# Performance work log

Measured on AMD Instinct MI355X. Metric: run time of the kernel, lower is better.

The kernel has to match this reference:

```python
import jax, jax.numpy as jnp
import numpy as np

VOCAB, D_MODEL, N_STATE, H_HEADS, LAYERS = 64, 512, 32, 16, 4
EXPAND = 2
D_INNER = EXPAND * D_MODEL          # 1024
P_HEAD = D_INNER // H_HEADS         # 64
CONV_DIM = D_INNER + 2 * N_STATE    # x, B, C share the depthwise conv
K_CONV = 4
D_IN_PROJ = 2 * D_INNER + 2 * N_STATE + H_HEADS  # z, x, B, C, dt
BATCH, SEQ = 4, 1024
EPS = 1e-5


def rmsnorm(x, w):
    return x * jax.lax.rsqrt(jnp.mean(x * x, axis=-1, keepdims=True) + EPS) * w


def silu(x):
    return x * jax.nn.sigmoid(x)


def causal_depthwise_conv(x, w, b):
    # x: [B,L,C], w: [C,K], b: [C]; causal (left) padding, depthwise groups
    xt = jnp.transpose(x, (0, 2, 1))  # [B,C,L]
    out = jax.lax.conv_general_dilated(xt, w[:, None, :], (1,), [(K_CONV - 1, 0)], feature_group_count=w.shape[0])
    return jnp.transpose(out, (0, 2, 1)) + b


def ssd(xh, dt, A, Bm, Cm, Dp):
    # Mamba2 SSD recurrence. xh [B,L,H,P], dt [B,L,H], A [H], Bm/Cm [B,L,N], Dp [H]
    dA = jnp.exp(dt * A)              # decay per (batch, step, head)
    dtx = dt[..., None] * xh          # [B,L,H,P]

    def step(h, inp):
        dA_t, dtx_t, B_t, C_t = inp
        # h: [B,H,P,N]
        h = dA_t[:, :, None, None] * h + dtx_t[..., None] * B_t[:, None, None, :]
        y = jnp.einsum('bhpn,bn->bhp', h, C_t)
        return h, y

    h0 = jnp.zeros((xh.shape[0], H_HEADS, P_HEAD, N_STATE), xh.dtype)
    _, ys = jax.lax.scan(step, h0, (jnp.moveaxis(dA, 1, 0), jnp.moveaxis(dtx, 1, 0), jnp.moveaxis(Bm, 1, 0), jnp.moveaxis(Cm, 1, 0)))
    return jnp.moveaxis(ys, 0, 1) + xh * Dp[None, None, :, None]


def mamba_block(x, norm_w, W_in, b_in, conv_w, conv_b, dt_bias, A_log, Dp, gnorm_w, W_out, b_out):
    res = x
    u = rmsnorm(x, norm_w)
    zxbcdt = u @ W_in + b_in                                # [B,L,D_IN_PROJ]
    z = zxbcdt[..., :D_INNER]
    xBC = zxbcdt[..., D_INNER:D_INNER + CONV_DIM]
    dt = zxbcdt[..., D_INNER + CONV_DIM:]                   # [B,L,H]
    xBC = silu(causal_depthwise_conv(xBC, conv_w, conv_b))
    xc = xBC[..., :D_INNER]
    Bm = xBC[..., D_INNER:D_INNER + N_STATE]
    Cm = xBC[..., D_INNER + N_STATE:]
    dt = jax.nn.softplus(dt + dt_bias)
    xh = xc.reshape(xc.shape[0], xc.shape[1], H_HEADS, P_HEAD)
    y = ssd(xh, dt, -jnp.exp(A_log), Bm, Cm, Dp)
    y = y.reshape(y.shape[0], y.shape[1], D_INNER)
    y = rmsnorm(y * silu(z), gnorm_w)                       # gated RMSNorm
    return res + y @ W_out + b_out


def forward(input_tokens, emb, norm_w, W_in, b_in, conv_w, conv_b, dt_bias, A_log, D_param, gnorm_w, W_out, b_out, head_w, head_b):
    h = emb[input_tokens]
    for i in range(LAYERS):
        h = mamba_block(h, norm_w[i], W_in[i], b_in[i], conv_w[i], conv_b[i], dt_bias[i], A_log[i], D_param[i], gnorm_w[i], W_out[i], b_out[i])
    return h @ head_w + head_b


def setup_inputs() -> dict:
    key = jax.random.key(0)
    ks = jax.random.split(key, 8)
    s = 0.02
    return {
        'input_tokens': jax.random.randint(ks[0], (BATCH, SEQ), 0, VOCAB),
        'emb': jax.random.normal(ks[1], (VOCAB, D_MODEL), jnp.float32) * s,
        'norm_w': jnp.ones((LAYERS, D_MODEL), jnp.float32),
        'W_in': jax.random.normal(ks[2], (LAYERS, D_MODEL, D_IN_PROJ), jnp.float32) * s,
        'b_in': jnp.zeros((LAYERS, D_IN_PROJ), jnp.float32),
        'conv_w': jax.random.normal(ks[3], (LAYERS, CONV_DIM, K_CONV), jnp.float32) * 0.1,
        'conv_b': jnp.zeros((LAYERS, CONV_DIM), jnp.float32),
        'dt_bias': jnp.tile(jnp.log(jnp.expm1(jnp.linspace(0.001, 0.1, H_HEADS, dtype=jnp.float32))), (LAYERS, 1)),
        'A_log': jnp.tile(jnp.log(jnp.arange(1, H_HEADS + 1, dtype=jnp.float32)), (LAYERS, 1)),
        'D_param': jnp.ones((LAYERS, H_HEADS), jnp.float32),
        'gnorm_w': jnp.ones((LAYERS, D_INNER), jnp.float32),
        'W_out': jax.random.normal(ks[4], (LAYERS, D_INNER, D_MODEL), jnp.float32) * s,
        'b_out': jnp.zeros((LAYERS, D_MODEL), jnp.float32),
        'head_w': jax.random.normal(ks[5], (D_MODEL, VOCAB), jnp.float32) * s,
        'head_b': jnp.zeros((VOCAB,), jnp.float32),
    }


def reference(input_tokens, emb, norm_w, W_in, b_in, conv_w, conv_b, dt_bias, A_log, D_param, gnorm_w, W_out, b_out, head_w, head_b):
    return forward(input_tokens, emb, norm_w, W_in, b_in, conv_w, conv_b, dt_bias, A_log, D_param, gnorm_w, W_out, b_out, head_w, head_b)
```

## Files before the change

### kernel.cpp

```cpp
#include <hip/hip_runtime.h>
#include <hip/hip_bf16.h>

#define VOCAB     64
#define D_MODEL   512
#define N_STATE   32
#define H_HEADS   16
#define LAYERS    4
#define D_INNER   1024
#define P_HEAD    64
#define CONV_DIM  1088
#define K_CONV    4
#define D_IN_PROJ 2128
#define NPAD_IN   2176
#define NPAD_HEAD 128
#define BATCH     4
#define SEQ       1024
#define NTOK      (BATCH*SEQ)
#define EPS       1e-5f
#define CL        64
#define NC        (SEQ/CL)
#define PSTR      80

typedef __bf16 bf16x8 __attribute__((ext_vector_type(8)));
typedef float  f32x4  __attribute__((ext_vector_type(4)));

__device__ __forceinline__ float sigmoidf_(float x) { return 1.f / (1.f + __expf(-x)); }
__device__ __forceinline__ float softplusf_(float x) { return (x > 20.f) ? x : log1pf(__expf(x)); }

__global__ void embed_kernel(const int* __restrict__ tok, const float* __restrict__ emb,
                             float* __restrict__ h) {
  int idx = blockIdx.x * 256 + threadIdx.x;
  if (idx >= NTOK * D_MODEL) return;
  int d = idx & (D_MODEL - 1);
  int t = idx >> 9;
  h[idx] = emb[tok[t] * D_MODEL + d];
}

__global__ void rmsnorm512_kernel(const float* __restrict__ x, const float* __restrict__ w,
                                  __bf16* __restrict__ out) {
  int tok = blockIdx.x;
  int tid = threadIdx.x;
  const float* xr = x + (size_t)tok * D_MODEL;
  float v0 = xr[tid], v1 = xr[tid + 256];
  float ss = v0 * v0 + v1 * v1;
  #pragma unroll
  for (int o = 32; o >= 1; o >>= 1) ss += __shfl_xor(ss, o);
  __shared__ float red[4];
  if ((tid & 63) == 0) red[tid >> 6] = ss;
  __syncthreads();
  float tot = red[0] + red[1] + red[2] + red[3];
  float sc = rsqrtf(tot * (1.f / D_MODEL) + EPS);
  out[(size_t)tok * D_MODEL + tid]       = (__bf16)(v0 * sc * w[tid]);
  out[(size_t)tok * D_MODEL + tid + 256] = (__bf16)(v1 * sc * w[tid + 256]);
}

__global__ void transpose_cast_kernel(const float* __restrict__ W, __bf16* __restrict__ Wt,
                                      int K, int N, int Npad) {
  W  += (size_t)blockIdx.z * K * N;
  Wt += (size_t)blockIdx.z * Npad * K;
  __shared__ float T[32][33];
  int n0 = blockIdx.x * 32, k0 = blockIdx.y * 32;
  int tx = threadIdx.x & 31, ty = threadIdx.x >> 5;
  #pragma unroll
  for (int i = 0; i < 4; i++) {
    int n = n0 + tx;
    T[ty + i * 8][tx] = (n < N) ? W[(size_t)(k0 + ty + i * 8) * N + n] : 0.f;
  }
  __syncthreads();
  #pragma unroll
  for (int i = 0; i < 4; i++)
    Wt[(size_t)(n0 + ty + i * 8) * K + k0 + tx] = (__bf16)T[tx][ty + i * 8];
}

#define TM 64
#define TN 128
#define TK 64
__global__ __launch_bounds__(256) void gemm_bf16_kernel(
    const __bf16* __restrict__ A, const __bf16* __restrict__ Bt,
    const float* __restrict__ bias, const float* __restrict__ res,
    float* __restrict__ C, __bf16* __restrict__ Cbf, int K, int N, int ldc) {
  __shared__ __bf16 As[TM * TK];
  __shared__ __bf16 Bs[TN * TK];
  int tid = threadIdx.x;
  int lane = tid & 63, wave = tid >> 6;
  int wm = wave >> 1, wn = wave & 1;
  int q = lane >> 4, l16 = lane & 15;
  size_t row0 = (size_t)blockIdx.y * TM;
  int col0 = blockIdx.x * TN;
  const __bf16* Ab = A + row0 * K;
  const __bf16* Bb = Bt + (size_t)col0 * K;

  bf16x8 pa[2], pb[4];
  #pragma unroll
  for (int r = 0; r < 2; r++) {
    int lin = r * 256 + tid;
    pa[r] = *(const bf16x8*)(Ab + (size_t)(lin >> 3) * K + (lin & 7) * 8);
  }
  #pragma unroll
  for (int r = 0; r < 4; r++) {
    int lin = r * 256 + tid;
    pb[r] = *(const bf16x8*)(Bb + (size_t)(lin >> 3) * K + (lin & 7) * 8);
  }

  f32x4 acc[2][4];
  #pragma unroll
  for (int i = 0; i < 2; i++)
    #pragma unroll
    for (int j = 0; j < 4; j++) acc[i][j] = (f32x4){0.f, 0.f, 0.f, 0.f};

  for (int k0 = 0; k0 < K; k0 += TK) {
    #pragma unroll
    for (int r = 0; r < 2; r++) { int lin = r * 256 + tid; *(bf16x8*)(As + lin * 8) = pa[r]; }
    #pragma unroll
    for (int r = 0; r < 4; r++) { int lin = r * 256 + tid; *(bf16x8*)(Bs + lin * 8) = pb[r]; }
    __syncthreads();
    int kn = k0 + TK;
    if (kn < K) {
      #pragma unroll
      for (int r = 0; r < 2; r++) {
        int lin = r * 256 + tid;
        pa[r] = *(const bf16x8*)(Ab + (size_t)(lin >> 3) * K + kn + (lin & 7) * 8);
      }
      #pragma unroll
      for (int r = 0; r < 4; r++) {
        int lin = r * 256 + tid;
        pb[r] = *(const bf16x8*)(Bb + (size_t)(lin >> 3) * K + kn + (lin & 7) * 8);
      }
    }
    #pragma unroll
    for (int ks = 0; ks < 2; ks++) {
      bf16x8 af[2], bfv[4];
      #pragma unroll
      for (int i = 0; i < 2; i++)
        af[i] = *(const bf16x8*)(As + (wm * 32 + i * 16 + l16) * TK + ks * 32 + q * 8);
      #pragma unroll
      for (int j = 0; j < 4; j++)
        bfv[j] = *(const bf16x8*)(Bs + (wn * 64 + j * 16 + l16) * TK + ks * 32 + q * 8);
      #pragma unroll
      for (int i = 0; i < 2; i++)
        #pragma unroll
        for (int j = 0; j < 4; j++)
          acc[i][j] = __builtin_amdgcn_mfma_f32_16x16x32_bf16(af[i], bfv[j], acc[i][j], 0, 0, 0);
    }
    __syncthreads();
  }

  #pragma unroll
  for (int i = 0; i < 2; i++) {
    size_t mrow = row0 + wm * 32 + i * 16 + q * 4;
    #pragma unroll
    for (int j = 0; j < 4; j++) {
      int col = col0 + wn * 64 + j * 16 + l16;
      if (col < N) {
        float bv = bias ? bias[col] : 0.f;
        #pragma unroll
        for (int rr = 0; rr < 4; rr++) {
          size_t off = (mrow + rr) * (size_t)ldc + col;
          float v = acc[i][j][rr] + bv;
          if (res) v += res[off];
          if (C)   C[off] = v;
          if (Cbf) Cbf[off] = (__bf16)v;
        }
      }
    }
  }
}

__global__ __launch_bounds__(256) void gemm_bf16_128(
    const __bf16* __restrict__ A, const __bf16* __restrict__ Bt,
    const float* __restrict__ bias, __bf16* __restrict__ Cbf,
    int K, int N, int ldc) {
  __shared__ __bf16 As[128 * TK];
  __shared__ __bf16 Bs[128 * TK];
  int tid = threadIdx.x;
  int lane = tid & 63, wave = tid >> 6;
  int wm = wave >> 1, wn = wave & 1;
  int q = lane >> 4, l16 = lane & 15;
  size_t row0 = (size_t)blockIdx.y * 128;
  int col0 = blockIdx.x * 128;
  const __bf16* Ab = A + row0 * K;
  const __bf16* Bb = Bt + (size_t)col0 * K;

  bf16x8 pa[4], pb[4];
  #pragma unroll
  for (int r = 0; r < 4; r++) {
    int lin = r * 256 + tid;
    pa[r] = *(const bf16x8*)(Ab + (size_t)(lin >> 3) * K + (lin & 7) * 8);
    pb[r] = *(const bf16x8*)(Bb + (size_t)(lin >> 3) * K + (lin & 7) * 8);
  }

  f32x4 acc[4][4];
  #pragma unroll
  for (int i = 0; i < 4; i++)
    #pragma unroll
    for (int j = 0; j < 4; j++) acc[i][j] = (f32x4){0.f, 0.f, 0.f, 0.f};

  for (int k0 = 0; k0 < K; k0 += TK) {
    #pragma unroll
    for (int r = 0; r < 4; r++) {
      int lin = r * 256 + tid;
      *(bf16x8*)(As + lin * 8) = pa[r];
      *(bf16x8*)(Bs + lin * 8) = pb[r];
    }
    __syncthreads();
    int kn = k0 + TK;
    if (kn < K) {
      #pragma unroll
      for (int r = 0; r < 4; r++) {
        int lin = r * 256 + tid;
        pa[r] = *(const bf16x8*)(Ab + (size_t)(lin >> 3) * K + kn + (lin & 7) * 8);
        pb[r] = *(const bf16x8*)(Bb + (size_t)(lin >> 3) * K + kn + (lin & 7) * 8);
      }
    }
    #pragma unroll
    for (int ks = 0; ks < 2; ks++) {
      bf16x8 af[4], bfv[4];
      #pragma unroll
      for (int i = 0; i < 4; i++)
        af[i] = *(const bf16x8*)(As + (wm * 64 + i * 16 + l16) * TK + ks * 32 + q * 8);
      #pragma unroll
      for (int j = 0; j < 4; j++)
        bfv[j] = *(const bf16x8*)(Bs + (wn * 64 + j * 16 + l16) * TK + ks * 32 + q * 8);
      #pragma unroll
      for (int i = 0; i < 4; i++)
        #pragma unroll
        for (int j = 0; j < 4; j++)
          acc[i][j] = __builtin_amdgcn_mfma_f32_16x16x32_bf16(af[i], bfv[j], acc[i][j], 0, 0, 0);
    }
    __syncthreads();
  }

  #pragma unroll
  for (int i = 0; i < 4; i++) {
    size_t mrow = row0 + wm * 64 + i * 16 + q * 4;
    #pragma unroll
    for (int j = 0; j < 4; j++) {
      int col = col0 + wn * 64 + j * 16 + l16;
      if (col < N) {
        float bv = bias[col];
        #pragma unroll
        for (int rr = 0; rr < 4; rr++)
          Cbf[(mrow + rr) * (size_t)ldc + col] = (__bf16)(acc[i][j][rr] + bv);
      }
    }
  }
}

__device__ __forceinline__ void wave0_dt_cumsum(
    const __bf16* __restrict__ zxbf, const float* __restrict__ dt_bias,
    int b, int h, int t0, int tid, float* ldt, float* lcs) {
  if (tid < 64) {
    float dv = (float)zxbf[((size_t)(b * SEQ + t0 + tid)) * D_IN_PROJ + 2 * D_INNER + 2 * N_STATE + h]
               + dt_bias[h];
    float dtv = softplusf_(dv);
    float cs = dtv;
    #pragma unroll
    for (int off = 1; off < 64; off <<= 1) {
      float o = __shfl_up(cs, off);
      if (tid >= off) cs += o;
    }
    ldt[tid] = dtv;
    lcs[tid] = cs;
  }
}

__global__ __launch_bounds__(256) void ssd_local_kernel(
    const __bf16* __restrict__ zxbf, const float* __restrict__ conv_w,
    const float* __restrict__ conv_b, const float* __restrict__ dt_bias,
    const float* __restrict__ A_log,
    float* __restrict__ Slocal, float* __restrict__ dAprod) {
  int blk = blockIdx.x;
  int c = blk % NC;
  int h = (blk / NC) % H_HEADS;
  int b = blk / (NC * H_HEADS);
  int tid = threadIdx.x;
  int lane = tid & 63, wave = tid >> 6;
  int q = lane >> 4, l16 = lane & 15;
  int t0 = c * CL;
  float A = -__expf(A_log[h]);
  __shared__ __bf16 rawx[68][64];
  __shared__ __bf16 rawB[68][32];
  __shared__ __bf16 lxT[64][PSTR];
  __shared__ __bf16 lBT[32][PSTR];
  __shared__ float ldt[64], lcs[64];
  for (int i = tid; i < 68 * 8; i += 256) {
    int r = i >> 3, c0 = (i & 7) * 8;
    int gr = t0 - 3 + r;
    bf16x8 v;
    #pragma unroll
    for (int k = 0; k < 8; k++) v[k] = (__bf16)0.f;
    if (gr >= 0)
      v = *(const bf16x8*)(zxbf + ((size_t)(b * SEQ + gr)) * D_IN_PROJ + D_INNER + h * 64 + c0);
    *(bf16x8*)(&rawx[r][c0]) = v;
  }
  for (int i = tid; i < 68 * 4; i += 256) {
    int r = i >> 2, c0 = (i & 3) * 8;
    int gr = t0 - 3 + r;
    bf16x8 v;
    #pragma unroll
    for (int k = 0; k < 8; k++) v[k] = (__bf16)0.f;
    if (gr >= 0)
      v = *(const bf16x8*)(zxbf + ((size_t)(b * SEQ + gr)) * D_IN_PROJ + 2 * D_INNER + c0);
    *(bf16x8*)(&rawB[r][c0]) = v;
  }
  wave0_dt_cumsum(zxbf, dt_bias, b, h, t0, tid, ldt, lcs);
  __syncthreads();
  float cs63 = lcs[63];
  {
    int p = tid & 63;
    const float* w = conv_w + (h * 64 + p) * K_CONV;
    float w0 = w[0], w1 = w[1], w2 = w[2], w3 = w[3];
    float cb = conv_b[h * 64 + p];
    for (int i = tid; i < CL * 64; i += 256) {
      int t = i >> 6;
      float a = cb + w0 * (float)rawx[t][p] + w1 * (float)rawx[t + 1][p]
                   + w2 * (float)rawx[t + 2][p] + w3 * (float)rawx[t + 3][p];
      lxT[p][t] = (__bf16)(a * sigmoidf_(a));
    }
  }
  {
    int n = tid & 31;
    const float* w = conv_w + (D_INNER + n) * K_CONV;
    float w0 = w[0], w1 = w[1], w2 = w[2], w3 = w[3];
    float cb = conv_b[D_INNER + n];
    for (int i = tid; i < CL * 32; i += 256) {
      int t = i >> 5;
      float a = cb + w0 * (float)rawB[t][n] + w1 * (float)rawB[t + 1][n]
                   + w2 * (float)rawB[t + 2][n] + w3 * (float)rawB[t + 3][n];
      float v = a * sigmoidf_(a);
      float wt = ldt[t] * __expf(A * (cs63 - lcs[t]));
      lBT[n][t] = (__bf16)(v * wt);
    }
  }
  __syncthreads();
  f32x4 acc[2];
  acc[0] = (f32x4){0.f,0.f,0.f,0.f}; acc[1] = (f32x4){0.f,0.f,0.f,0.f};
  #pragma unroll
  for (int kb = 0; kb < 2; kb++) {
    bf16x8 af = *(const bf16x8*)(&lxT[wave * 16 + l16][kb * 32 + q * 8]);
    #pragma unroll
    for (int j = 0; j < 2; j++) {
      bf16x8 bf = *(const bf16x8*)(&lBT[l16 + 16 * j][kb * 32 + q * 8]);
      acc[j] = __builtin_amdgcn_mfma_f32_16x16x32_bf16(af, bf, acc[j], 0, 0, 0);
    }
  }
  float* dst = Slocal + (size_t)blk * 2048;
  #pragma unroll
  for (int j = 0; j < 2; j++) {
    int n = l16 + 16 * j;
    #pragma unroll
    for (int rr = 0; rr < 4; rr++) {
      int p = wave * 16 + q * 4 + rr;
      dst[p * 32 + n] = acc[j][rr];
    }
  }
  if (tid == 0) dAprod[blk] = __expf(A * cs63);
}

__global__ __launch_bounds__(256) void ssd_combine_kernel(
    float* __restrict__ S, const float* __restrict__ dAprod) {
  int bh = blockIdx.x >> 1;
  int half = blockIdx.x & 1;
  __shared__ float pr[NC];
  if (threadIdx.x < NC) pr[threadIdx.x] = dAprod[bh * NC + threadIdx.x];
  __syncthreads();
  float* base = S + (size_t)bh * NC * 2048 + half * 1024 + threadIdx.x * 4;
  f32x4 tmp[NC];
  #pragma unroll
  for (int c = 0; c < NC; c++) tmp[c] = *(const f32x4*)(base + c * 2048);
  f32x4 st = (f32x4){0.f, 0.f, 0.f, 0.f};
  #pragma unroll
  for (int c = 0; c < NC; c++) {
    f32x4 cur = tmp[c];
    *(f32x4*)(base + c * 2048) = st;
    st = pr[c] * st + cur;
  }
}

__global__ __launch_bounds__(256) void ssd_out_kernel(
    const __bf16* __restrict__ zxbf, const float* __restrict__ conv_w,
    const float* __restrict__ conv_b, const float* __restrict__ dt_bias,
    const float* __restrict__ A_log, const float* __restrict__ Dp,
    const float* __restrict__ Sstart, __bf16* __restrict__ y) {
  int blk = blockIdx.x;
  int c = blk % NC;
  int h = (blk / NC) % H_HEADS;
  int b = blk / (NC * H_HEADS);
  int tid = threadIdx.x;
  int lane = tid & 63, wave = tid >> 6;
  int q = lane >> 4, l16 = lane & 15;
  int t0 = c * CL;
  float A = -__expf(A_log[h]);
  float D = Dp[h];
  __shared__ __bf16 rawbuf[2 * 68 * 64];
  __shared__ __bf16 lxT[64][PSTR];
  __shared__ __bf16 lB[64][32];
  __shared__ __bf16 lC[64][32];
  __shared__ __bf16 lS[64][32];
  __shared__ float ldt[64], lcs[64];
  __bf16* rawx = rawbuf;
  __bf16* rawBC = rawbuf + 68 * 64;
  for (int i = tid; i < 68 * 8; i += 256) {
    int r = i >> 3, c0 = (i & 7) * 8;
    int gr = t0 - 3 + r;
    bf16x8 vx, vbc;
    #pragma unroll
    for (int k = 0; k < 8; k++) { vx[k] = (__bf16)0.f; vbc[k] = (__bf16)0.f; }
    if (gr >= 0) {
      const __bf16* rowp = zxbf + ((size_t)(b * SEQ + gr)) * D_IN_PROJ;
      vx  = *(const bf16x8*)(rowp + D_INNER + h * 64 + c0);
      vbc = *(const bf16x8*)(rowp + 2 * D_INNER + c0);
    }
    *(bf16x8*)(rawx + r * 64 + c0)  = vx;
    *(bf16x8*)(rawBC + r * 64 + c0) = vbc;
  }
  wave0_dt_cumsum(zxbf, dt_bias, b, h, t0, tid, ldt, lcs);
  __syncthreads();
  {
    int p = tid & 63;
    const float* w = conv_w + (h * 64 + p) * K_CONV;
    float w0 = w[0], w1 = w[1], w2 = w[2], w3 = w[3];
    float cb = conv_b[h * 64 + p];
    for (int i = tid; i < CL * 64; i += 256) {
      int t = i >> 6;
      float a = cb + w0 * (float)rawx[t * 64 + p] + w1 * (float)rawx[(t + 1) * 64 + p]
                   + w2 * (float)rawx[(t + 2) * 64 + p] + w3 * (float)rawx[(t + 3) * 64 + p];
      lxT[p][t] = (__bf16)(a * sigmoidf_(a));
    }
  }
  {
    int col = tid & 63;
    const float* w = conv_w + (D_INNER + col) * K_CONV;
    float w0 = w[0], w1 = w[1], w2 = w[2], w3 = w[3];
    float cb = conv_b[D_INNER + col];
    for (int i = tid; i < CL * 64; i += 256) {
      int t = i >> 6;
      float a = cb + w0 * (float)rawBC[t * 64 + col] + w1 * (float)rawBC[(t + 1) * 64 + col]
                   + w2 * (float)rawBC[(t + 2) * 64 + col] + w3 * (float)rawBC[(t + 3) * 64 + col];
      float v = a * sigmoidf_(a);
      if (col < 32) lB[t][col] = (__bf16)v; else lC[t][col - 32] = (__bf16)v;
    }
  }
  {
    const float* src = Sstart + (size_t)blk * 2048;
    for (int i = tid; i < 2048; i += 256) lS[i >> 5][i & 31] = (__bf16)src[i];
  }
  __syncthreads();
  bf16x8 afC = *(const bf16x8*)(&lC[wave * 16 + l16][q * 8]);
  f32x4 accG[4], accI[4], accY[4];
  #pragma unroll
  for (int j = 0; j < 4; j++) {
    accG[j] = (f32x4){0.f,0.f,0.f,0.f};
    accI[j] = (f32x4){0.f,0.f,0.f,0.f};
    accY[j] = (f32x4){0.f,0.f,0.f,0.f};
  }
  #pragma unroll
  for (int j = 0; j < 4; j++) {
    bf16x8 bf = *(const bf16x8*)(&lB[l16 + 16 * j][q * 8]);
    accG[j] = __builtin_amdgcn_mfma_f32_16x16x32_bf16(afC, bf, accG[j], 0, 0, 0);
  }
  #pragma unroll
  for (int j = 0; j < 4; j++) {
    bf16x8 bf = *(const bf16x8*)(&lS[l16 + 16 * j][q * 8]);
    accI[j] = __builtin_amdgcn_mfma_f32_16x16x32_bf16(afC, bf, accI[j], 0, 0, 0);
  }
  __bf16* pP = rawbuf + wave * 16 * PSTR;
  #pragma unroll
  for (int j = 0; j < 4; j++) {
    int s = l16 + 16 * j;
    float css = lcs[s], dts = ldt[s];
    #pragma unroll
    for (int rr = 0; rr < 4; rr++) {
      int tl = q * 4 + rr;
      int t = wave * 16 + tl;
      float val = accG[j][rr] * __expf(A * (lcs[t] - css)) * dts;
      if (s == t) val += D;
      if (s > t) val = 0.f;
      pP[tl * PSTR + s] = (__bf16)val;
    }
  }
  #pragma unroll
  for (int kb = 0; kb < 2; kb++) {
    bf16x8 afP = *(const bf16x8*)(pP + l16 * PSTR + kb * 32 + q * 8);
    #pragma unroll
    for (int j = 0; j < 4; j++) {
      bf16x8 bf = *(const bf16x8*)(&lxT[l16 + 16 * j][kb * 32 + q * 8]);
      accY[j] = __builtin_amdgcn_mfma_f32_16x16x32_bf16(afP, bf, accY[j], 0, 0, 0);
    }
  }
  #pragma unroll
  for (int rr = 0; rr < 4; rr++) {
    int t = wave * 16 + q * 4 + rr;
    float cumt = __expf(A * lcs[t]);
    __bf16* yrow = y + ((size_t)(b * SEQ + t0 + t)) * D_INNER + h * 64;
    #pragma unroll
    for (int j = 0; j < 4; j++) {
      int p = l16 + 16 * j;
      yrow[p] = (__bf16)(accY[j][rr] + cumt * accI[j][rr]);
    }
  }
}

__global__ void gate_norm_kernel(const __bf16* __restrict__ zxbf, const float* __restrict__ gw,
                                 const __bf16* __restrict__ y, __bf16* __restrict__ ybf) {
  int tok = blockIdx.x;
  int tid = threadIdx.x;
  const __bf16* zr = zxbf + (size_t)tok * D_IN_PROJ;
  const __bf16* yr = y + (size_t)tok * D_INNER;
  float v[4];
  float ss = 0.f;
  #pragma unroll
  for (int i = 0; i < 4; i++) {
    int d = tid + i * 256;
    float z = (float)zr[d];
    float g = (float)yr[d] * z * sigmoidf_(z);
    v[i] = g;
    ss += g * g;
  }
  #pragma unroll
  for (int o = 32; o >= 1; o >>= 1) ss += __shfl_xor(ss, o);
  __shared__ float red[4];
  if ((tid & 63) == 0) red[tid >> 6] = ss;
  __syncthreads();
  float tot = red[0] + red[1] + red[2] + red[3];
  float sc = rsqrtf(tot * (1.f / D_INNER) + EPS);
  #pragma unroll
  for (int i = 0; i < 4; i++) {
    int d = tid + i * 256;
    ybf[(size_t)tok * D_INNER + d] = (__bf16)(v[i] * sc * gw[d]);
  }
}

extern "C" void kernel_launch(void* const* d_in, const int* in_sizes, int n_in,
                              void* d_out, int out_size, void* d_ws, size_t ws_size,
                              hipStream_t stream) {
  const int*   tok     = (const int*)  d_in[0];
  const float* emb     = (const float*)d_in[1];
  const float* norm_w  = (const float*)d_in[2];
  const float* W_in    = (const float*)d_in[3];
  const float* b_in    = (const float*)d_in[4];
  const float* conv_w  = (const float*)d_in[5];
  const float* conv_b  = (const float*)d_in[6];
  const float* dt_bias = (const float*)d_in[7];
  const float* A_log   = (const float*)d_in[8];
  const float* D_par   = (const float*)d_in[9];
  const float* gnorm_w = (const float*)d_in[10];
  const float* W_out   = (const float*)d_in[11];
  const float* b_out   = (const float*)d_in[12];
  const float* head_w  = (const float*)d_in[13];
  const float* head_b  = (const float*)d_in[14];
  float* out = (float*)d_out;

  char* p = (char*)d_ws;
  auto alloc = [&](size_t bytes) { void* r = (void*)p; p += (bytes + 255) & ~(size_t)255; return r; };
  float*  h      = (float*) alloc((size_t)NTOK * D_MODEL * 4);
  float*  slocal = (float*) alloc((size_t)BATCH * H_HEADS * NC * P_HEAD * N_STATE * 4);
  float*  daprod = (float*) alloc((size_t)BATCH * H_HEADS * NC * 4);
  __bf16* y      = (__bf16*)alloc((size_t)NTOK * D_INNER * 2);
  __bf16* zxbf   = (__bf16*)alloc((size_t)NTOK * D_IN_PROJ * 2);
  __bf16* ubf    = (__bf16*)alloc((size_t)NTOK * D_MODEL * 2);
  __bf16* ybf    = (__bf16*)alloc((size_t)NTOK * D_INNER * 2);
  __bf16* hbf    = (__bf16*)alloc((size_t)NTOK * D_MODEL * 2);
  __bf16* WtIn   = (__bf16*)alloc((size_t)LAYERS * NPAD_IN * D_MODEL * 2);
  __bf16* WtOut  = (__bf16*)alloc((size_t)LAYERS * D_MODEL * D_INNER * 2);
  __bf16* WtHead = (__bf16*)alloc((size_t)NPAD_HEAD * D_MODEL * 2);

  transpose_cast_kernel<<<dim3(NPAD_IN / 32, D_MODEL / 32, LAYERS), 256, 0, stream>>>(
      W_in, WtIn, D_MODEL, D_IN_PROJ, NPAD_IN);
  transpose_cast_kernel<<<dim3(D_MODEL / 32, D_INNER / 32, LAYERS), 256, 0, stream>>>(
      W_out, WtOut, D_INNER, D_MODEL, D_MODEL);
  transpose_cast_kernel<<<dim3(NPAD_HEAD / 32, D_MODEL / 32, 1), 256, 0, stream>>>(
      head_w, WtHead, D_MODEL, VOCAB, NPAD_HEAD);

  embed_kernel<<<(NTOK * D_MODEL + 255) / 256, 256, 0, stream>>>(tok, emb, h);

  for (int l = 0; l < LAYERS; l++) {
    rmsnorm512_kernel<<<NTOK, 256, 0, stream>>>(h, norm_w + (size_t)l * D_MODEL, ubf);

    gemm_bf16_128<<<dim3(NPAD_IN / 128, NTOK / 128), 256, 0, stream>>>(
        ubf, WtIn + (size_t)l * NPAD_IN * D_MODEL, b_in + (size_t)l * D_IN_PROJ,
        zxbf, D_MODEL, D_IN_PROJ, D_IN_PROJ);

    ssd_local_kernel<<<BATCH * H_HEADS * NC, 256, 0, stream>>>(
        zxbf, conv_w + (size_t)l * CONV_DIM * K_CONV, conv_b + (size_t)l * CONV_DIM,
        dt_bias + (size_t)l * H_HEADS, A_log + (size_t)l * H_HEADS, slocal, daprod);
    ssd_combine_kernel<<<BATCH * H_HEADS * 2, 256, 0, stream>>>(slocal, daprod);
    ssd_out_kernel<<<BATCH * H_HEADS * NC, 256, 0, stream>>>(
        zxbf, conv_w + (size_t)l * CONV_DIM * K_CONV, conv_b + (size_t)l * CONV_DIM,
        dt_bias + (size_t)l * H_HEADS, A_log + (size_t)l * H_HEADS,
        D_par + (size_t)l * H_HEADS, slocal, y);

    gate_norm_kernel<<<NTOK, 256, 0, stream>>>(zxbf, gnorm_w + (size_t)l * D_INNER, y, ybf);

    gemm_bf16_kernel<<<dim3(D_MODEL / TN, NTOK / TM), 256, 0, stream>>>(
        ybf, WtOut + (size_t)l * D_MODEL * D_INNER, b_out + (size_t)l * D_MODEL, h, h,
        (l == LAYERS - 1) ? hbf : nullptr, D_INNER, D_MODEL, D_MODEL);
  }

  gemm_bf16_kernel<<<dim3(NPAD_HEAD / TN, NTOK / TM), 256, 0, stream>>>(
      hbf, WtHead, head_b, nullptr, out, nullptr, D_MODEL, VOCAB, VOCAB);
}
```

Before: 497.7 us.

## Cache conv outputs from SSD local pass and fuse embedding into first rmsnorm

The SSD local kernel now writes its post-conv x, B/C tiles and dt/cumsum values to global scratch buffers. The SSD output kernel reads these directly instead of reloading raw zxbf, recomputing the depthwise conv and SiLU, and staging through shared memory. The embedding lookup is folded into the first layer's rmsnorm kernel, which removes one launch. In exchange there are extra global writes and reads of the per-chunk tiles, and the out kernel now does uncoalesced per-lane global fragment loads with an in-register fp32-to-bf16 cast of the state.

```diff
diff --git a/kernel.cpp b/kernel.cpp
--- a/kernel.cpp
+++ b/kernel.cpp
@@ -27,21 +27,22 @@
 __device__ __forceinline__ float sigmoidf_(float x) { return 1.f / (1.f + __expf(-x)); }
 __device__ __forceinline__ float softplusf_(float x) { return (x > 20.f) ? x : log1pf(__expf(x)); }
 
-__global__ void embed_kernel(const int* __restrict__ tok, const float* __restrict__ emb,
-                             float* __restrict__ h) {
-  int idx = blockIdx.x * 256 + threadIdx.x;
-  if (idx >= NTOK * D_MODEL) return;
-  int d = idx & (D_MODEL - 1);
-  int t = idx >> 9;
-  h[idx] = emb[tok[t] * D_MODEL + d];
-}
-
 __global__ void rmsnorm512_kernel(const float* __restrict__ x, const float* __restrict__ w,
-                                  __bf16* __restrict__ out) {
-  int tok = blockIdx.x;
+                                  __bf16* __restrict__ out,
+                                  const int* __restrict__ tok, const float* __restrict__ emb,
+                                  float* __restrict__ hout) {
+  int tokid = blockIdx.x;
   int tid = threadIdx.x;
-  const float* xr = x + (size_t)tok * D_MODEL;
-  float v0 = xr[tid], v1 = xr[tid + 256];
+  float v0, v1;
+  if (tok) {
+    const float* er = emb + (size_t)tok[tokid] * D_MODEL;
+    v0 = er[tid]; v1 = er[tid + 256];
+    float* hr = hout + (size_t)tokid * D_MODEL;
+    hr[tid] = v0; hr[tid + 256] = v1;
+  } else {
+    const float* xr = x + (size_t)tokid * D_MODEL;
+    v0 = xr[tid]; v1 = xr[tid + 256];
+  }
   float ss = v0 * v0 + v1 * v1;
   #pragma unroll
   for (int o = 32; o >= 1; o >>= 1) ss += __shfl_xor(ss, o);
@@ -50,8 +51,8 @@
   __syncthreads();
   float tot = red[0] + red[1] + red[2] + red[3];
   float sc = rsqrtf(tot * (1.f / D_MODEL) + EPS);
-  out[(size_t)tok * D_MODEL + tid]       = (__bf16)(v0 * sc * w[tid]);
-  out[(size_t)tok * D_MODEL + tid + 256] = (__bf16)(v1 * sc * w[tid + 256]);
+  out[(size_t)tokid * D_MODEL + tid]       = (__bf16)(v0 * sc * w[tid]);
+  out[(size_t)tokid * D_MODEL + tid + 256] = (__bf16)(v1 * sc * w[tid + 256]);
 }
 
 __global__ void transpose_cast_kernel(const float* __restrict__ W, __bf16* __restrict__ Wt,
@@ -268,7 +269,8 @@
     const __bf16* __restrict__ zxbf, const float* __restrict__ conv_w,
     const float* __restrict__ conv_b, const float* __restrict__ dt_bias,
     const float* __restrict__ A_log,
-    float* __restrict__ Slocal, float* __restrict__ dAprod) {
+    float* __restrict__ Slocal, float* __restrict__ dAprod,
+    __bf16* __restrict__ gx, __bf16* __restrict__ gbc, float* __restrict__ gdtcs) {
   int blk = blockIdx.x;
   int c = blk % NC;
   int h = (blk / NC) % H_HEADS;
@@ -279,29 +281,24 @@
   int t0 = c * CL;
   float A = -__expf(A_log[h]);
   __shared__ __bf16 rawx[68][64];
-  __shared__ __bf16 rawB[68][32];
+  __shared__ __bf16 rawBC[68][64];
   __shared__ __bf16 lxT[64][PSTR];
   __shared__ __bf16 lBT[32][PSTR];
+  __shared__ __bf16 lBC[64][64];
   __shared__ float ldt[64], lcs[64];
   for (int i = tid; i < 68 * 8; i += 256) {
     int r = i >> 3, c0 = (i & 7) * 8;
     int gr = t0 - 3 + r;
-    bf16x8 v;
-    #pragma unroll
-    for (int k = 0; k < 8; k++) v[k] = (__bf16)0.f;
-    if (gr >= 0)
-      v = *(const bf16x8*)(zxbf + ((size_t)(b * SEQ + gr)) * D_IN_PROJ + D_INNER + h * 64 + c0);
-    *(bf16x8*)(&rawx[r][c0]) = v;
-  }
-  for (int i = tid; i < 68 * 4; i += 256) {
-    int r = i >> 2, c0 = (i & 3) * 8;
-    int gr = t0 - 3 + r;
-    bf16x8 v;
-    #pragma unroll
-    for (int k = 0; k < 8; k++) v[k] = (__bf16)0.f;
-    if (gr >= 0)
-      v = *(const bf16x8*)(zxbf + ((size_t)(b * SEQ + gr)) * D_IN_PROJ + 2 * D_INNER + c0);
-    *(bf16x8*)(&rawB[r][c0]) = v;
+    bf16x8 vx, vbc;
+    #pragma unroll
+    for (int k = 0; k < 8; k++) { vx[k] = (__bf16)0.f; vbc[k] = (__bf16)0.f; }
+    if (gr >= 0) {
+      const __bf16* rowp = zxbf + ((size_t)(b * SEQ + gr)) * D_IN_PROJ;
+      vx  = *(const bf16x8*)(rowp + D_INNER + h * 64 + c0);
+      vbc = *(const bf16x8*)(rowp + 2 * D_INNER + c0);
+    }
+    *(bf16x8*)(&rawx[r][c0])  = vx;
+    *(bf16x8*)(&rawBC[r][c0]) = vbc;
   }
   wave0_dt_cumsum(zxbf, dt_bias, b, h, t0, tid, ldt, lcs);
   __syncthreads();
@@ -319,17 +316,20 @@
     }
   }
   {
-    int n = tid & 31;
-    const float* w = conv_w + (D_INNER + n) * K_CONV;
+    int col = tid & 63;
+    const float* w = conv_w + (D_INNER + col) * K_CONV;
     float w0 = w[0], w1 = w[1], w2 = w[2], w3 = w[3];
-    float cb = conv_b[D_INNER + n];
-    for (int i = tid; i < CL * 32; i += 256) {
-      int t = i >> 5;
-      float a = cb + w0 * (float)rawB[t][n] + w1 * (float)rawB[t + 1][n]
-                   + w2 * (float)rawB[t + 2][n] + w3 * (float)rawB[t + 3][n];
+    float cb = conv_b[D_INNER + col];
+    for (int i = tid; i < CL * 64; i += 256) {
+      int t = i >> 6;
+      float a = cb + w0 * (float)rawBC[t][col] + w1 * (float)rawBC[t + 1][col]
+                   + w2 * (float)rawBC[t + 2][col] + w3 * (float)rawBC[t + 3][col];
       float v = a * sigmoidf_(a);
-      float wt = ldt[t] * __expf(A * (cs63 - lcs[t]));
-      lBT[n][t] = (__bf16)(v * wt);
+      lBC[t][col] = (__bf16)v;
+      if (col < 32) {
+        float wt = ldt[t] * __expf(A * (cs63 - lcs[t]));
+        lBT[col][t] = (__bf16)(v * wt);
+      }
     }
   }
   __syncthreads();
@@ -353,6 +353,19 @@
       int p = wave * 16 + q * 4 + rr;
       dst[p * 32 + n] = acc[j][rr];
     }
+  }
+  {
+    __bf16* gxb = gx + (size_t)blk * 4096;
+    __bf16* gbcb = gbc + (size_t)blk * 4096;
+    #pragma unroll
+    for (int r = 0; r < 2; r++) {
+      int i = r * 256 + tid;
+      int p = i >> 3, t8 = (i & 7) * 8;
+      *(bf16x8*)(gxb + p * 64 + t8)  = *(const bf16x8*)(&lxT[p][t8]);
+      *(bf16x8*)(gbcb + p * 64 + t8) = *(const bf16x8*)(&lBC[p][t8]);
+    }
+    for (int i = tid; i < 128; i += 256)
+      gdtcs[(size_t)blk * 128 + i] = (i < 64) ? ldt[i] : lcs[i - 64];
   }
   if (tid == 0) dAprod[blk] = __expf(A * cs63);
 }
@@ -378,8 +391,8 @@
 }
 
 __global__ __launch_bounds__(256) void ssd_out_kernel(
-    const __bf16* __restrict__ zxbf, const float* __restrict__ conv_w,
-    const float* __restrict__ conv_b, const float* __restrict__ dt_bias,
+    const __bf16* __restrict__ gx, const __bf16* __restrict__ gbc,
+    const float* __restrict__ gdtcs,
     const float* __restrict__ A_log, const float* __restrict__ Dp,
     const float* __restrict__ Sstart, __bf16* __restrict__ y) {
   int blk = blockIdx.x;
@@ -392,61 +405,17 @@
   int t0 = c * CL;
   float A = -__expf(A_log[h]);
   float D = Dp[h];
-  __shared__ __bf16 rawbuf[2 * 68 * 64];
-  __shared__ __bf16 lxT[64][PSTR];
-  __shared__ __bf16 lB[64][32];
-  __shared__ __bf16 lC[64][32];
-  __shared__ __bf16 lS[64][32];
+  __shared__ __bf16 pP[4 * 16 * PSTR];
   __shared__ float ldt[64], lcs[64];
-  __bf16* rawx = rawbuf;
-  __bf16* rawBC = rawbuf + 68 * 64;
-  for (int i = tid; i < 68 * 8; i += 256) {
-    int r = i >> 3, c0 = (i & 7) * 8;
-    int gr = t0 - 3 + r;
-    bf16x8 vx, vbc;
-    #pragma unroll
-    for (int k = 0; k < 8; k++) { vx[k] = (__bf16)0.f; vbc[k] = (__bf16)0.f; }
-    if (gr >= 0) {
-      const __bf16* rowp = zxbf + ((size_t)(b * SEQ + gr)) * D_IN_PROJ;
-      vx  = *(const bf16x8*)(rowp + D_INNER + h * 64 + c0);
-      vbc = *(const bf16x8*)(rowp + 2 * D_INNER + c0);
-    }
-    *(bf16x8*)(rawx + r * 64 + c0)  = vx;
-    *(bf16x8*)(rawBC + r * 64 + c0) = vbc;
-  }
-  wave0_dt_cumsum(zxbf, dt_bias, b, h, t0, tid, ldt, lcs);
-  __syncthreads();
-  {
-    int p = tid & 63;
-    const float* w = conv_w + (h * 64 + p) * K_CONV;
-    float w0 = w[0], w1 = w[1], w2 = w[2], w3 = w[3];
-    float cb = conv_b[h * 64 + p];
-    for (int i = tid; i < CL * 64; i += 256) {
-      int t = i >> 6;
-      float a = cb + w0 * (float)rawx[t * 64 + p] + w1 * (float)rawx[(t + 1) * 64 + p]
-                   + w2 * (float)rawx[(t + 2) * 64 + p] + w3 * (float)rawx[(t + 3) * 64 + p];
-      lxT[p][t] = (__bf16)(a * sigmoidf_(a));
-    }
-  }
-  {
-    int col = tid & 63;
-    const float* w = conv_w + (D_INNER + col) * K_CONV;
-    float w0 = w[0], w1 = w[1], w2 = w[2], w3 = w[3];
-    float cb = conv_b[D_INNER + col];
-    for (int i = tid; i < CL * 64; i += 256) {
-      int t = i >> 6;
-      float a = cb + w0 * (float)rawBC[t * 64 + col] + w1 * (float)rawBC[(t + 1) * 64 + col]
-                   + w2 * (float)rawBC[(t + 2) * 64 + col] + w3 * (float)rawBC[(t + 3) * 64 + col];
-      float v = a * sigmoidf_(a);
-      if (col < 32) lB[t][col] = (__bf16)v; else lC[t][col - 32] = (__bf16)v;
-    }
-  }
-  {
-    const float* src = Sstart + (size_t)blk * 2048;
-    for (int i = tid; i < 2048; i += 256) lS[i >> 5][i & 31] = (__bf16)src[i];
-  }
-  __syncthreads();
-  bf16x8 afC = *(const bf16x8*)(&lC[wave * 16 + l16][q * 8]);
+  if (tid < 128) {
+    float v = gdtcs[(size_t)blk * 128 + tid];
+    if (tid < 64) ldt[tid] = v; else lcs[tid - 64] = v;
+  }
+  const __bf16* xt = gx + (size_t)blk * 4096;
+  const __bf16* bc = gbc + (size_t)blk * 4096;
+  const float*  ss = Sstart + (size_t)blk * 2048;
+
+  bf16x8 afC = *(const bf16x8*)(bc + (wave * 16 + l16) * 64 + 32 + q * 8);
   f32x4 accG[4], accI[4], accY[4];
   #pragma unroll
   for (int j = 0; j < 4; j++) {
@@ -456,15 +425,21 @@
   }
   #pragma unroll
   for (int j = 0; j < 4; j++) {
-    bf16x8 bf = *(const bf16x8*)(&lB[l16 + 16 * j][q * 8]);
+    bf16x8 bf = *(const bf16x8*)(bc + (l16 + 16 * j) * 64 + q * 8);
     accG[j] = __builtin_amdgcn_mfma_f32_16x16x32_bf16(afC, bf, accG[j], 0, 0, 0);
   }
   #pragma unroll
   for (int j = 0; j < 4; j++) {
-    bf16x8 bf = *(const bf16x8*)(&lS[l16 + 16 * j][q * 8]);
+    const float* sp = ss + (l16 + 16 * j) * 32 + q * 8;
+    f32x4 a = *(const f32x4*)(sp);
+    f32x4 bq = *(const f32x4*)(sp + 4);
+    bf16x8 bf;
+    #pragma unroll
+    for (int k = 0; k < 4; k++) { bf[k] = (__bf16)a[k]; bf[4 + k] = (__bf16)bq[k]; }
     accI[j] = __builtin_amdgcn_mfma_f32_16x16x32_bf16(afC, bf, accI[j], 0, 0, 0);
   }
-  __bf16* pP = rawbuf + wave * 16 * PSTR;
+  __syncthreads();
+  __bf16* pPw = pP + wave * 16 * PSTR;
   #pragma unroll
   for (int j = 0; j < 4; j++) {
     int s = l16 + 16 * j;
@@ -476,15 +451,15 @@
       float val = accG[j][rr] * __expf(A * (lcs[t] - css)) * dts;
       if (s == t) val += D;
       if (s > t) val = 0.f;
-      pP[tl * PSTR + s] = (__bf16)val;
+      pPw[tl * PSTR + s] = (__bf16)val;
     }
   }
   #pragma unroll
   for (int kb = 0; kb < 2; kb++) {
-    bf16x8 afP = *(const bf16x8*)(pP + l16 * PSTR + kb * 32 + q * 8);
+    bf16x8 afP = *(const bf16x8*)(pPw + l16 * PSTR + kb * 32 + q * 8);
     #pragma unroll
     for (int j = 0; j < 4; j++) {
-      bf16x8 bf = *(const bf16x8*)(&lxT[l16 + 16 * j][kb * 32 + q * 8]);
+      bf16x8 bf = *(const bf16x8*)(xt + (l16 + 16 * j) * 64 + kb * 32 + q * 8);
       accY[j] = __builtin_amdgcn_mfma_f32_16x16x32_bf16(afP, bf, accY[j], 0, 0, 0);
     }
   }
@@ -556,6 +531,9 @@
   float*  h      = (float*) alloc((size_t)NTOK * D_MODEL * 4);
   float*  slocal = (float*) alloc((size_t)BATCH * H_HEADS * NC * P_HEAD * N_STATE * 4);
   float*  daprod = (float*) alloc((size_t)BATCH * H_HEADS * NC * 4);
+  float*  gdtcs  = (float*) alloc((size_t)BATCH * H_HEADS * NC * 128 * 4);
+  __bf16* gx     = (__bf16*)alloc((size_t)BATCH * H_HEADS * NC * 4096 * 2);
+  __bf16* gbc    = (__bf16*)alloc((size_t)BATCH * H_HEADS * NC * 4096 * 2);
   __bf16* y      = (__bf16*)alloc((size_t)NTOK * D_INNER * 2);
   __bf16* zxbf   = (__bf16*)alloc((size_t)NTOK * D_IN_PROJ * 2);
   __bf16* ubf    = (__bf16*)alloc((size_t)NTOK * D_MODEL * 2);
@@ -572,10 +550,10 @@
   transpose_cast_kernel<<<dim3(NPAD_HEAD / 32, D_MODEL / 32, 1), 256, 0, stream>>>(
       head_w, WtHead, D_MODEL, VOCAB, NPAD_HEAD);
 
-  embed_kernel<<<(NTOK * D_MODEL + 255) / 256, 256, 0, stream>>>(tok, emb, h);
-
   for (int l = 0; l < LAYERS; l++) {
-    rmsnorm512_kernel<<<NTOK, 256, 0, stream>>>(h, norm_w + (size_t)l * D_MODEL, ubf);
+    rmsnorm512_kernel<<<NTOK, 256, 0, stream>>>(
+        h, norm_w + (size_t)l * D_MODEL, ubf,
+        (l == 0) ? tok : nullptr, (l == 0) ? emb : nullptr, h);
 
     gemm_bf16_128<<<dim3(NPAD_IN / 128, NTOK / 128), 256, 0, stream>>>(
         ubf, WtIn + (size_t)l * NPAD_IN * D_MODEL, b_in + (size_t)l * D_IN_PROJ,
@@ -583,11 +561,11 @@
 
     ssd_local_kernel<<<BATCH * H_HEADS * NC, 256, 0, stream>>>(
         zxbf, conv_w + (size_t)l * CONV_DIM * K_CONV, conv_b + (size_t)l * CONV_DIM,
-        dt_bias + (size_t)l * H_HEADS, A_log + (size_t)l * H_HEADS, slocal, daprod);
+        dt_bias + (size_t)l * H_HEADS, A_log + (size_t)l * H_HEADS,
+        slocal, daprod, gx, gbc, gdtcs);
     ssd_combine_kernel<<<BATCH * H_HEADS * 2, 256, 0, stream>>>(slocal, daprod);
     ssd_out_kernel<<<BATCH * H_HEADS * NC, 256, 0, stream>>>(
-        zxbf, conv_w + (size_t)l * CONV_DIM * K_CONV, conv_b + (size_t)l * CONV_DIM,
-        dt_bias + (size_t)l * H_HEADS, A_log + (size_t)l * H_HEADS,
+        gx, gbc, gdtcs, A_log + (size_t)l * H_HEADS,
         D_par + (size_t)l * H_HEADS, slocal, y);
 
     gate_norm_kernel<<<NTOK, 256, 0, stream>>>(zxbf, gnorm_w + (size_t)l * D_INNER, y, ybf);
```

After: 516.7 us. +3.8%, slower.

## Fuse chunk-state combine into SSD output kernel and embed into first rmsnorm

Applied to the files above, without the earlier changes.

Removes the separate ssd_combine kernel. Each ssd_out block now rebuilds its starting state by scanning the local states of all earlier chunks with the decay products. The embedding gather is also folded into the first layer's rmsnorm launch, which drops two launches per forward pass. The trade is redundant work: late chunks reread up to 15 chunk states, which is quadratic in chunk count, instead of one linear pass.

```diff
diff --git a/kernel.cpp b/kernel.cpp
--- a/kernel.cpp
+++ b/kernel.cpp
@@ -27,21 +27,22 @@
 __device__ __forceinline__ float sigmoidf_(float x) { return 1.f / (1.f + __expf(-x)); }
 __device__ __forceinline__ float softplusf_(float x) { return (x > 20.f) ? x : log1pf(__expf(x)); }
 
-__global__ void embed_kernel(const int* __restrict__ tok, const float* __restrict__ emb,
-                             float* __restrict__ h) {
-  int idx = blockIdx.x * 256 + threadIdx.x;
-  if (idx >= NTOK * D_MODEL) return;
-  int d = idx & (D_MODEL - 1);
-  int t = idx >> 9;
-  h[idx] = emb[tok[t] * D_MODEL + d];
-}
-
 __global__ void rmsnorm512_kernel(const float* __restrict__ x, const float* __restrict__ w,
-                                  __bf16* __restrict__ out) {
-  int tok = blockIdx.x;
+                                  __bf16* __restrict__ out,
+                                  const int* __restrict__ tok, const float* __restrict__ emb,
+                                  float* __restrict__ hout) {
+  int tokid = blockIdx.x;
   int tid = threadIdx.x;
-  const float* xr = x + (size_t)tok * D_MODEL;
-  float v0 = xr[tid], v1 = xr[tid + 256];
+  float v0, v1;
+  if (tok) {
+    const float* er = emb + (size_t)tok[tokid] * D_MODEL;
+    v0 = er[tid]; v1 = er[tid + 256];
+    float* hr = hout + (size_t)tokid * D_MODEL;
+    hr[tid] = v0; hr[tid + 256] = v1;
+  } else {
+    const float* xr = x + (size_t)tokid * D_MODEL;
+    v0 = xr[tid]; v1 = xr[tid + 256];
+  }
   float ss = v0 * v0 + v1 * v1;
   #pragma unroll
   for (int o = 32; o >= 1; o >>= 1) ss += __shfl_xor(ss, o);
@@ -50,8 +51,8 @@
   __syncthreads();
   float tot = red[0] + red[1] + red[2] + red[3];
   float sc = rsqrtf(tot * (1.f / D_MODEL) + EPS);
-  out[(size_t)tok * D_MODEL + tid]       = (__bf16)(v0 * sc * w[tid]);
-  out[(size_t)tok * D_MODEL + tid + 256] = (__bf16)(v1 * sc * w[tid + 256]);
+  out[(size_t)tokid * D_MODEL + tid]       = (__bf16)(v0 * sc * w[tid]);
+  out[(size_t)tokid * D_MODEL + tid + 256] = (__bf16)(v1 * sc * w[tid + 256]);
 }
 
 __global__ void transpose_cast_kernel(const float* __restrict__ W, __bf16* __restrict__ Wt,
@@ -357,31 +358,12 @@
   if (tid == 0) dAprod[blk] = __expf(A * cs63);
 }
 
-__global__ __launch_bounds__(256) void ssd_combine_kernel(
-    float* __restrict__ S, const float* __restrict__ dAprod) {
-  int bh = blockIdx.x >> 1;
-  int half = blockIdx.x & 1;
-  __shared__ float pr[NC];
-  if (threadIdx.x < NC) pr[threadIdx.x] = dAprod[bh * NC + threadIdx.x];
-  __syncthreads();
-  float* base = S + (size_t)bh * NC * 2048 + half * 1024 + threadIdx.x * 4;
-  f32x4 tmp[NC];
-  #pragma unroll
-  for (int c = 0; c < NC; c++) tmp[c] = *(const f32x4*)(base + c * 2048);
-  f32x4 st = (f32x4){0.f, 0.f, 0.f, 0.f};
-  #pragma unroll
-  for (int c = 0; c < NC; c++) {
-    f32x4 cur = tmp[c];
-    *(f32x4*)(base + c * 2048) = st;
-    st = pr[c] * st + cur;
-  }
-}
-
 __global__ __launch_bounds__(256) void ssd_out_kernel(
     const __bf16* __restrict__ zxbf, const float* __restrict__ conv_w,
     const float* __restrict__ conv_b, const float* __restrict__ dt_bias,
     const float* __restrict__ A_log, const float* __restrict__ Dp,
-    const float* __restrict__ Sstart, __bf16* __restrict__ y) {
+    const float* __restrict__ Slocal, const float* __restrict__ dAprod,
+    __bf16* __restrict__ y) {
   int blk = blockIdx.x;
   int c = blk % NC;
   int h = (blk / NC) % H_HEADS;
@@ -398,6 +380,7 @@
   __shared__ __bf16 lC[64][32];
   __shared__ __bf16 lS[64][32];
   __shared__ float ldt[64], lcs[64];
+  __shared__ float pr[NC];
   __bf16* rawx = rawbuf;
   __bf16* rawBC = rawbuf + 68 * 64;
   for (int i = tid; i < 68 * 8; i += 256) {
@@ -414,6 +397,7 @@
     *(bf16x8*)(rawx + r * 64 + c0)  = vx;
     *(bf16x8*)(rawBC + r * 64 + c0) = vbc;
   }
+  if (tid < NC) pr[tid] = dAprod[(blk - c) + tid];
   wave0_dt_cumsum(zxbf, dt_bias, b, h, t0, tid, ldt, lcs);
   __syncthreads();
   {
@@ -442,8 +426,18 @@
     }
   }
   {
-    const float* src = Sstart + (size_t)blk * 2048;
-    for (int i = tid; i < 2048; i += 256) lS[i >> 5][i & 31] = (__bf16)src[i];
+    int p = tid >> 2, n0 = (tid & 3) * 8;
+    const float* sl = Slocal + (size_t)(blk - c) * 2048 + p * 32 + n0;
+    float st[8] = {};
+    for (int j = 0; j < c; j++) {
+      f32x4 a = *(const f32x4*)(sl + (size_t)j * 2048);
+      f32x4 bq = *(const f32x4*)(sl + (size_t)j * 2048 + 4);
+      float prj = pr[j];
+      #pragma unroll
+      for (int k = 0; k < 4; k++) { st[k] = prj * st[k] + a[k]; st[4 + k] = prj * st[4 + k] + bq[k]; }
+    }
+    #pragma unroll
+    for (int k = 0; k < 8; k++) lS[p][n0 + k] = (__bf16)st[k];
   }
   __syncthreads();
   bf16x8 afC = *(const bf16x8*)(&lC[wave * 16 + l16][q * 8]);
@@ -572,10 +566,10 @@
   transpose_cast_kernel<<<dim3(NPAD_HEAD / 32, D_MODEL / 32, 1), 256, 0, stream>>>(
       head_w, WtHead, D_MODEL, VOCAB, NPAD_HEAD);
 
-  embed_kernel<<<(NTOK * D_MODEL + 255) / 256, 256, 0, stream>>>(tok, emb, h);
-
   for (int l = 0; l < LAYERS; l++) {
-    rmsnorm512_kernel<<<NTOK, 256, 0, stream>>>(h, norm_w + (size_t)l * D_MODEL, ubf);
+    rmsnorm512_kernel<<<NTOK, 256, 0, stream>>>(
+        h, norm_w + (size_t)l * D_MODEL, ubf,
+        (l == 0) ? tok : nullptr, (l == 0) ? emb : nullptr, h);
 
     gemm_bf16_128<<<dim3(NPAD_IN / 128, NTOK / 128), 256, 0, stream>>>(
         ubf, WtIn + (size_t)l * NPAD_IN * D_MODEL, b_in + (size_t)l * D_IN_PROJ,
@@ -584,11 +578,10 @@
     ssd_local_kernel<<<BATCH * H_HEADS * NC, 256, 0, stream>>>(
         zxbf, conv_w + (size_t)l * CONV_DIM * K_CONV, conv_b + (size_t)l * CONV_DIM,
         dt_bias + (size_t)l * H_HEADS, A_log + (size_t)l * H_HEADS, slocal, daprod);
-    ssd_combine_kernel<<<BATCH * H_HEADS * 2, 256, 0, stream>>>(slocal, daprod);
     ssd_out_kernel<<<BATCH * H_HEADS * NC, 256, 0, stream>>>(
         zxbf, conv_w + (size_t)l * CONV_DIM * K_CONV, conv_b + (size_t)l * CONV_DIM,
         dt_bias + (size_t)l * H_HEADS, A_log + (size_t)l * H_HEADS,
-        D_par + (size_t)l * H_HEADS, slocal, y);
+        D_par + (size_t)l * H_HEADS, slocal, daprod, y);
 
     gate_norm_kernel<<<NTOK, 256, 0, stream>>>(zxbf, gnorm_w + (size_t)l * D_INNER, y, ybf);
 
```

After: 494.4 us, median of 2. Within noise of the previous version (-0.7%).
